# Kernel tuning notes

Measured on AMD Instinct MI355X. Metric: run time of the kernel, lower is better.

The kernel has to match this reference:

```python
import jax, jax.numpy as jnp
import numpy as np

N_NODES = 100000
N_EDGES = 1600000
IN_DIM = 128
HIDDEN = 128
OUT_DIM = 64


def setup_inputs() -> dict:
    key = jax.random.key(0)
    ks = jax.random.split(key, 10)
    s = 0.05
    return {
        "x": jax.random.normal(ks[0], (N_NODES, IN_DIM), jnp.float32),
        "edge_index": jax.random.randint(ks[1], (2, N_EDGES), 0, N_NODES, dtype=jnp.int64),
        "w_l0": jax.random.normal(ks[2], (IN_DIM, HIDDEN), jnp.float32) * s,
        "b_l0": jnp.zeros((HIDDEN,), jnp.float32),
        "w_r0": jax.random.normal(ks[3], (IN_DIM, HIDDEN), jnp.float32) * s,
        "w_l1": jax.random.normal(ks[4], (HIDDEN, HIDDEN), jnp.float32) * s,
        "b_l1": jnp.zeros((HIDDEN,), jnp.float32),
        "w_r1": jax.random.normal(ks[5], (HIDDEN, HIDDEN), jnp.float32) * s,
        "w_out": jax.random.normal(ks[6], (HIDDEN, OUT_DIM), jnp.float32) * s,
        "b_out": jnp.zeros((OUT_DIM,), jnp.float32),
    }


def _sage_conv(x, src, dst, w_l, b_l, w_r, num_nodes):
    # mean-aggregate source features at destination nodes (PyG SAGEConv, aggr='mean')
    msgs = x[src]                                             # [E, D] gather
    agg = jax.ops.segment_sum(msgs, dst, num_segments=num_nodes)
    deg = jax.ops.segment_sum(jnp.ones((src.shape[0],), x.dtype), dst,
                              num_segments=num_nodes)
    agg = agg / jnp.maximum(deg, 1.0)[:, None]                # isolated nodes -> 0
    return agg @ w_l + b_l + x @ w_r


def reference(x, edge_index, w_l0, b_l0, w_r0, w_l1, b_l1, w_r1, w_out, b_out):
    src, dst = edge_index[0], edge_index[1]
    n = x.shape[0]
    h = jax.nn.relu(_sage_conv(x, src, dst, w_l0, b_l0, w_r0, n))
    h = jax.nn.relu(_sage_conv(h, src, dst, w_l1, b_l1, w_r1, n))
    return jax.nn.sigmoid(h @ w_out + b_out)
```

## Files before the change

### kernel.cpp

```cpp
#include <hip/hip_runtime.h>
#include <hip/hip_bf16.h>
#include <cstdint>

#define N_NODES 100000
#define N_EDGES 1600000
#define DIM 128
#define K2 256
#define ODIM 64
#define NPB 64
#define CB 98
#define NREP 8
#define CAP1 2560
#define EPB 4096

typedef __hip_bfloat16 bf16;
typedef __attribute__((ext_vector_type(8))) short bfrag;
typedef __attribute__((ext_vector_type(4))) float f32x4;
typedef __attribute__((ext_vector_type(2))) float f32x2;

__global__ __launch_bounds__(1024) void k_bucket(const int* __restrict__ src,
                                                 const int* __restrict__ dst,
                                                 int* __restrict__ gcur,
                                                 uint32_t* __restrict__ bdata) {
  __shared__ int hist[CB], hbase[CB], hcur[CB], gstart[CB];
  __shared__ uint32_t ent[EPB];
  __shared__ uint8_t kslot[EPB];
  const int tid = threadIdx.x;
  const int rep = blockIdx.x & (NREP - 1);
  const int e0 = blockIdx.x * EPB;
  const int cnt = min(EPB, N_EDGES - e0);

  if (tid < CB) { hist[tid] = 0; hcur[tid] = 0; }
  __syncthreads();

  const int me0 = e0 + tid * 4;
  int ss[4], dd[4];
  int nmine = max(0, min(4, N_EDGES - me0));
  if (nmine == 4) {
    *(int4*)ss = *(const int4*)(src + me0);
    *(int4*)dd = *(const int4*)(dst + me0);
  } else {
    for (int q = 0; q < nmine; ++q) { ss[q] = src[me0 + q]; dd[q] = dst[me0 + q]; }
  }

#pragma unroll
  for (int q = 0; q < 4; ++q)
    if (q < nmine) atomicAdd(&hist[dd[q] >> 10], 1);
  __syncthreads();

  if (tid == 0) {
    int run = 0;
    for (int b = 0; b < CB; ++b) { hbase[b] = run; run += hist[b]; }
  }
  __syncthreads();

#pragma unroll
  for (int q = 0; q < 4; ++q)
    if (q < nmine) {
      int key = dd[q] >> 10;
      int r = atomicAdd(&hcur[key], 1);
      int p = hbase[key] + r;
      ent[p] = ((uint32_t)ss[q] << 10) | (uint32_t)(dd[q] & 1023);
      kslot[p] = (uint8_t)key;
    }
  __syncthreads();

  if (tid < CB && hist[tid] > 0)
    gstart[tid] = atomicAdd(&gcur[rep * CB + tid], hist[tid]);
  __syncthreads();

  for (int i = tid; i < cnt; i += 1024) {
    int k = kslot[i];
    int pos = gstart[k] + (i - hbase[k]);
    if (pos < CAP1)
      bdata[((size_t)(rep * CB + k)) * CAP1 + pos] = ent[i];
  }
}

__global__ __launch_bounds__(256) void k_csr(const uint32_t* __restrict__ bdata,
                                             const int* __restrict__ gcur,
                                             int* __restrict__ rowptr,
                                             int* __restrict__ col) {
  __shared__ int nc[1024], noff[1024];
  __shared__ int red[256];
  __shared__ int sz[NREP];
  const int b = blockIdx.x, tid = threadIdx.x;

  if (tid < NREP) sz[tid] = min(gcur[tid * CB + b], CAP1);

  int part = 0;
  for (int i = tid; i < NREP * b; i += 256) {
    int bp = i >> 3, r = i & 7;
    part += min(gcur[r * CB + bp], CAP1);
  }
  red[tid] = part;
  __syncthreads();
  for (int off = 128; off > 0; off >>= 1) {
    if (tid < off) red[tid] += red[tid + off];
    __syncthreads();
  }
  const int base = red[0];
  __syncthreads();

  for (int i = tid; i < 1024; i += 256) nc[i] = 0;
  __syncthreads();

  for (int r = 0; r < NREP; ++r) {
    int c = sz[r];
    const uint32_t* seg = bdata + ((size_t)(r * CB + b)) * CAP1;
    for (int i = tid; i < c; i += 256)
      atomicAdd(&nc[seg[i] & 1023], 1);
  }
  __syncthreads();

  int loc[4], s = 0;
#pragma unroll
  for (int q = 0; q < 4; ++q) { loc[q] = nc[tid * 4 + q]; s += loc[q]; }
  red[tid] = s;
  __syncthreads();
  for (int off = 1; off < 256; off <<= 1) {
    int add = (tid >= off) ? red[tid - off] : 0;
    __syncthreads();
    red[tid] += add;
    __syncthreads();
  }
  int p = red[tid] - s;
#pragma unroll
  for (int q = 0; q < 4; ++q) { noff[tid * 4 + q] = p; p += loc[q]; }
  __syncthreads();

  for (int i = tid; i < 1024; i += 256) {
    int n = b * 1024 + i;
    if (n < N_NODES) rowptr[n] = base + noff[i];
  }
  if (b == 0 && tid == 0) rowptr[N_NODES] = N_EDGES;

  for (int i = tid; i < 1024; i += 256) nc[i] = 0;
  __syncthreads();

  for (int r = 0; r < NREP; ++r) {
    int c = sz[r];
    const uint32_t* seg = bdata + ((size_t)(r * CB + b)) * CAP1;
    for (int i = tid; i < c; i += 256) {
      uint32_t e = seg[i];
      int n = e & 1023;
      int pos = atomicAdd(&nc[n], 1);
      col[base + noff[n] + pos] = (int)((e >> 10) << 7);
    }
  }
}

__global__ __launch_bounds__(256) void k_cvt(const float* __restrict__ x,
                                             bf16* __restrict__ xb,
                                             uint8_t* __restrict__ x8) {
  int i = (blockIdx.x * 256 + threadIdx.x) * 4;
  if (i >= N_NODES * DIM) return;
  float4 v = *(const float4*)(x + i);
  bf16 t[4];
  t[0] = __float2bfloat16(v.x);
  t[1] = __float2bfloat16(v.y);
  t[2] = __float2bfloat16(v.z);
  t[3] = __float2bfloat16(v.w);
  *(uint2*)(xb + i) = *(uint2*)t;
  int p8 = __builtin_amdgcn_cvt_pk_fp8_f32(v.x, v.y, 0, false);
  p8 = __builtin_amdgcn_cvt_pk_fp8_f32(v.z, v.w, p8, true);
  *(int*)(x8 + i) = p8;
}

__global__ __launch_bounds__(256) void k_cvt8(const bf16* __restrict__ h,
                                              uint8_t* __restrict__ h8) {
  int i = (blockIdx.x * 256 + threadIdx.x) * 8;
  if (i >= N_NODES * DIM) return;
  uint4 v = *(const uint4*)(h + i);
  uint32_t ws[4] = {v.x, v.y, v.z, v.w};
  float f[8];
#pragma unroll
  for (int q = 0; q < 4; ++q) {
    f[2 * q]     = __uint_as_float(ws[q] << 16);
    f[2 * q + 1] = __uint_as_float(ws[q] & 0xFFFF0000u);
  }
  int lo = __builtin_amdgcn_cvt_pk_fp8_f32(f[0], f[1], 0, false);
  lo = __builtin_amdgcn_cvt_pk_fp8_f32(f[2], f[3], lo, true);
  int hi = __builtin_amdgcn_cvt_pk_fp8_f32(f[4], f[5], 0, false);
  hi = __builtin_amdgcn_cvt_pk_fp8_f32(f[6], f[7], hi, true);
  uint2 o; o.x = (uint32_t)lo; o.y = (uint32_t)hi;
  *(uint2*)(h8 + i) = o;
}

__global__ __launch_bounds__(256) void k_prepw(const float* __restrict__ wl0,
                                               const float* __restrict__ wr0,
                                               const float* __restrict__ wl1,
                                               const float* __restrict__ wr1,
                                               const float* __restrict__ wo,
                                               bf16* __restrict__ WT0,
                                               bf16* __restrict__ WT1,
                                               bf16* __restrict__ WoT) {
  int g = blockIdx.x * 256 + threadIdx.x;
  if (g < 32768) {
    int j = g >> 8, k = g & 255;
    float v = (k < DIM) ? wl0[k * DIM + j] : wr0[(k - DIM) * DIM + j];
    WT0[g] = __float2bfloat16(v);
  } else if (g < 65536) {
    int gg = g - 32768;
    int j = gg >> 8, k = gg & 255;
    float v = (k < DIM) ? wl1[k * DIM + j] : wr1[(k - DIM) * DIM + j];
    WT1[gg] = __float2bfloat16(v);
  } else if (g < 65536 + 8192) {
    int gg = g - 65536;
    int j = gg >> 7, k = gg & 127;
    WoT[gg] = __float2bfloat16(wo[k * ODIM + j]);
  }
}

__device__ __forceinline__ void accv8(f32x2* acc, uint2 v) {
  f32x2 t0 = __builtin_amdgcn_cvt_pk_f32_fp8(v.x, false);
  f32x2 t1 = __builtin_amdgcn_cvt_pk_f32_fp8(v.x, true);
  f32x2 t2 = __builtin_amdgcn_cvt_pk_f32_fp8(v.y, false);
  f32x2 t3 = __builtin_amdgcn_cvt_pk_f32_fp8(v.y, true);
  acc[0] += t0; acc[1] += t1; acc[2] += t2; acc[3] += t3;
}

__global__ __launch_bounds__(256) void k_agg(const uint8_t* __restrict__ feat8,
                                             const int* __restrict__ rowptr,
                                             const int* __restrict__ colb,
                                             bf16* __restrict__ agg) {
  int gid = blockIdx.x * 256 + threadIdx.x;
  int node = gid >> 6;
  if (node >= N_NODES) return;
  int lane = gid & 63;
  int g = lane >> 4, lg = lane & 15;
  int beg = rowptr[node], end = rowptr[node + 1];
  const char* fb = (const char*)feat8 + lg * 8;

  f32x2 acc[4];
#pragma unroll
  for (int q = 0; q < 4; ++q) acc[q] = (f32x2){0.f, 0.f};

  int j = beg;
  for (; j + 16 <= end; j += 16) {
    int o0 = colb[j + g];
    int o1 = colb[j + 4 + g];
    int o2 = colb[j + 8 + g];
    int o3 = colb[j + 12 + g];
    uint2 v0 = *(const uint2*)(fb + o0);
    uint2 v1 = *(const uint2*)(fb + o1);
    uint2 v2 = *(const uint2*)(fb + o2);
    uint2 v3 = *(const uint2*)(fb + o3);
    accv8(acc, v0); accv8(acc, v1); accv8(acc, v2); accv8(acc, v3);
  }
  for (; j + 4 <= end; j += 4) {
    int o = colb[j + g];
    uint2 v = *(const uint2*)(fb + o);
    accv8(acc, v);
  }
  int rem = end - j;
  if (g < rem) {
    int o = colb[j + g];
    uint2 v = *(const uint2*)(fb + o);
    accv8(acc, v);
  }

#pragma unroll
  for (int q = 0; q < 4; ++q) {
#pragma unroll
    for (int c = 0; c < 2; ++c) {
      acc[q][c] += __shfl_xor(acc[q][c], 16, 64);
      acc[q][c] += __shfl_xor(acc[q][c], 32, 64);
    }
  }

  if (g == 0) {
    float inv = (end > beg) ? 1.0f / (float)(end - beg) : 0.f;
    union { uint32_t u[4]; uint4 v; } o;
#pragma unroll
    for (int q = 0; q < 4; ++q) {
      __hip_bfloat162 h;
      h.x = __float2bfloat16(acc[q][0] * inv);
      h.y = __float2bfloat16(acc[q][1] * inv);
      o.u[q] = *(uint32_t*)&h;
    }
    *(uint4*)(agg + (size_t)node * DIM + lg * 8) = o.v;
  }
}

__global__ __launch_bounds__(256) void k_sage(const bf16* __restrict__ agg,
                                              const bf16* __restrict__ xb,
                                              const bf16* __restrict__ WT,
                                              const float* __restrict__ bias,
                                              bf16* __restrict__ hout) {
  __shared__ char sA[NPB * 512];
  const int tid = threadIdx.x;
  const int base = blockIdx.x * NPB;

#pragma unroll
  for (int i = 0; i < 8; ++i) {
    int c = tid + 256 * i;
    int row = c >> 5, kc = c & 31;
    int n = base + row;
    uint4 v = make_uint4(0, 0, 0, 0);
    if (n < N_NODES) {
      const bf16* sp = (kc < 16) ? (agg + (size_t)n * DIM + kc * 8)
                                 : (xb + (size_t)n * DIM + (kc - 16) * 8);
      v = *(const uint4*)sp;
    }
    int byte = (row * 512 + kc * 16) ^ ((row & 7) << 4);
    *(uint4*)(sA + byte) = v;
  }
  __syncthreads();

  const int w = tid >> 6, lane = tid & 63;
  const int j0 = w * 32;
  const int lrow = lane & 15, lk = lane >> 4;

  f32x4 acc[4][2];
#pragma unroll
  for (int mi = 0; mi < 4; ++mi)
#pragma unroll
    for (int ni = 0; ni < 2; ++ni)
      acc[mi][ni] = (f32x4){0.f, 0.f, 0.f, 0.f};

  for (int kt = 0; kt < 8; ++kt) {
    bfrag b0 = *(const bfrag*)(WT + (size_t)(j0 + lrow) * K2 + kt * 32 + lk * 8);
    bfrag b1 = *(const bfrag*)(WT + (size_t)(j0 + 16 + lrow) * K2 + kt * 32 + lk * 8);
#pragma unroll
    for (int mi = 0; mi < 4; ++mi) {
      int row = mi * 16 + lrow;
      int byte = (row * 512 + kt * 64 + lk * 16) ^ ((row & 7) << 4);
      bfrag a = *(const bfrag*)(sA + byte);
      acc[mi][0] = __builtin_amdgcn_mfma_f32_16x16x32_bf16(a, b0, acc[mi][0], 0, 0, 0);
      acc[mi][1] = __builtin_amdgcn_mfma_f32_16x16x32_bf16(a, b1, acc[mi][1], 0, 0, 0);
    }
  }

#pragma unroll
  for (int ni = 0; ni < 2; ++ni) {
    int colj = j0 + ni * 16 + lrow;
    float bv = bias[colj];
#pragma unroll
    for (int mi = 0; mi < 4; ++mi) {
#pragma unroll
      for (int r = 0; r < 4; ++r) {
        int n = base + mi * 16 + lk * 4 + r;
        if (n < N_NODES)
          hout[(size_t)n * DIM + colj] = __float2bfloat16(fmaxf(acc[mi][ni][r] + bv, 0.f));
      }
    }
  }
}

__global__ __launch_bounds__(256) void k_out(const bf16* __restrict__ agg,
                                             const bf16* __restrict__ xb,
                                             const bf16* __restrict__ WT,
                                             const float* __restrict__ bias,
                                             const bf16* __restrict__ WoT,
                                             const float* __restrict__ bo,
                                             float* __restrict__ out) {
  __shared__ char sA[NPB * 512];
  const int tid = threadIdx.x;
  const int base = blockIdx.x * NPB;

#pragma unroll
  for (int i = 0; i < 8; ++i) {
    int c = tid + 256 * i;
    int row = c >> 5, kc = c & 31;
    int n = base + row;
    uint4 v = make_uint4(0, 0, 0, 0);
    if (n < N_NODES) {
      const bf16* sp = (kc < 16) ? (agg + (size_t)n * DIM + kc * 8)
                                 : (xb + (size_t)n * DIM + (kc - 16) * 8);
      v = *(const uint4*)sp;
    }
    int byte = (row * 512 + kc * 16) ^ ((row & 7) << 4);
    *(uint4*)(sA + byte) = v;
  }
  __syncthreads();

  const int w = tid >> 6, lane = tid & 63;
  const int j0 = w * 32;
  const int lrow = lane & 15, lk = lane >> 4;

  f32x4 acc[4][2];
#pragma unroll
  for (int mi = 0; mi < 4; ++mi)
#pragma unroll
    for (int ni = 0; ni < 2; ++ni)
      acc[mi][ni] = (f32x4){0.f, 0.f, 0.f, 0.f};

  for (int kt = 0; kt < 8; ++kt) {
    bfrag b0 = *(const bfrag*)(WT + (size_t)(j0 + lrow) * K2 + kt * 32 + lk * 8);
    bfrag b1 = *(const bfrag*)(WT + (size_t)(j0 + 16 + lrow) * K2 + kt * 32 + lk * 8);
#pragma unroll
    for (int mi = 0; mi < 4; ++mi) {
      int row = mi * 16 + lrow;
      int byte = (row * 512 + kt * 64 + lk * 16) ^ ((row & 7) << 4);
      bfrag a = *(const bfrag*)(sA + byte);
      acc[mi][0] = __builtin_amdgcn_mfma_f32_16x16x32_bf16(a, b0, acc[mi][0], 0, 0, 0);
      acc[mi][1] = __builtin_amdgcn_mfma_f32_16x16x32_bf16(a, b1, acc[mi][1], 0, 0, 0);
    }
  }

  __syncthreads();
#pragma unroll
  for (int ni = 0; ni < 2; ++ni) {
    int colj = j0 + ni * 16 + lrow;
    float bv = bias[colj];
#pragma unroll
    for (int mi = 0; mi < 4; ++mi) {
#pragma unroll
      for (int r = 0; r < 4; ++r) {
        int row = mi * 16 + lk * 4 + r;
        float v = fmaxf(acc[mi][ni][r] + bv, 0.f);
        int byte = (row * 256 + colj * 2) ^ ((row & 7) << 4);
        *(bf16*)(sA + byte) = __float2bfloat16(v);
      }
    }
  }
  __syncthreads();

  const int jo = w * 16;
  f32x4 acc2[4];
#pragma unroll
  for (int mi = 0; mi < 4; ++mi) acc2[mi] = (f32x4){0.f, 0.f, 0.f, 0.f};

#pragma unroll
  for (int kt = 0; kt < 4; ++kt) {
    bfrag b = *(const bfrag*)(WoT + (size_t)(jo + lrow) * DIM + kt * 32 + lk * 8);
#pragma unroll
    for (int mi = 0; mi < 4; ++mi) {
      int row = mi * 16 + lrow;
      int byte = (row * 256 + kt * 64 + lk * 16) ^ ((row & 7) << 4);
      bfrag a = *(const bfrag*)(sA + byte);
      acc2[mi] = __builtin_amdgcn_mfma_f32_16x16x32_bf16(a, b, acc2[mi], 0, 0, 0);
    }
  }

  int colj = jo + lrow;
  float bv = bo[colj];
#pragma unroll
  for (int mi = 0; mi < 4; ++mi) {
#pragma unroll
    for (int r = 0; r < 4; ++r) {
      int n = base + mi * 16 + lk * 4 + r;
      if (n < N_NODES)
        out[(size_t)n * ODIM + colj] = 1.f / (1.f + __expf(-(acc2[mi][r] + bv)));
    }
  }
}

extern "C" void kernel_launch(void* const* d_in, const int* in_sizes, int n_in,
                              void* d_out, int out_size, void* d_ws, size_t ws_size,
                              hipStream_t stream) {
  const float* x     = (const float*)d_in[0];
  const int*   ei    = (const int*)d_in[1];
  const float* w_l0  = (const float*)d_in[2];
  const float* b_l0  = (const float*)d_in[3];
  const float* w_r0  = (const float*)d_in[4];
  const float* w_l1  = (const float*)d_in[5];
  const float* b_l1  = (const float*)d_in[6];
  const float* w_r1  = (const float*)d_in[7];
  const float* w_out = (const float*)d_in[8];
  const float* b_out = (const float*)d_in[9];
  float* out = (float*)d_out;

  const int* src = ei;
  const int* dst = ei + N_EDGES;

  char* ws = (char*)d_ws;
  int*      rowptr = (int*)(ws);
  int*      gcur   = (int*)(ws + (512u << 10));
  int*      col    = (int*)(ws + (1u << 20));
  uint32_t* bdata  = (uint32_t*)(ws + (8u << 20));
  uint8_t*  x8     = (uint8_t*)(ws + (8u << 20));
  uint8_t*  h08    = (uint8_t*)(ws + (8u << 20));
  bf16*     WT0    = (bf16*)(ws + (21u << 20));
  bf16*     WT1    = (bf16*)(ws + (21u << 20) + 65536);
  bf16*     WoT    = (bf16*)(ws + (21u << 20) + 131072);
  bf16*     aggb   = (bf16*)(ws + (22ull << 20));
  bf16*     h0b    = (bf16*)(ws + (48ull << 20));
  bf16*     xb     = (bf16*)(ws + (74ull << 20));

  hipMemsetAsync(gcur, 0, NREP * CB * sizeof(int), stream);
  k_bucket<<<(N_EDGES + EPB - 1) / EPB, 1024, 0, stream>>>(src, dst, gcur, bdata);
  k_csr   <<<CB, 256, 0, stream>>>(bdata, gcur, rowptr, col);

  k_cvt  <<<(N_NODES * DIM / 4 + 255) / 256, 256, 0, stream>>>(x, xb, x8);
  k_prepw<<<(65536 + 8192 + 255) / 256, 256, 0, stream>>>(w_l0, w_r0, w_l1, w_r1, w_out,
                                                          WT0, WT1, WoT);

  const int ablocks = (N_NODES * 64 + 255) / 256;
  const int gblocks = (N_NODES + NPB - 1) / NPB;

  k_agg <<<ablocks, 256, 0, stream>>>(x8, rowptr, col, aggb);
  k_sage<<<gblocks, 256, 0, stream>>>(aggb, xb, WT0, b_l0, h0b);

  k_cvt8<<<(N_NODES * DIM / 8 + 255) / 256, 256, 0, stream>>>(h0b, h08);
  k_agg <<<ablocks, 256, 0, stream>>>(h08, rowptr, col, aggb);
  k_out <<<gblocks, 256, 0, stream>>>(aggb, h0b, WT1, b_l1, WoT, b_out, out);
}
```

Before: 238.8 us.

## Fuse fp8 conversion into sage epilogue, use direct LDS loads, per-wave histograms

Removes the separate k_cvt8 kernel by having k_sage write the fp8 copy of the hidden layer alongside the bf16 output. The A-tile staging in k_sage and k_out now uses global_load_lds to copy straight into shared memory, folding the XOR swizzle into the source address. k_bucket switches to per-wave histograms and cursors to reduce LDS atomic contention. The trade-offs are byte-wide scattered fp8 stores in the epilogue and clamped duplicate loads for tail rows.

```diff
diff --git a/kernel.cpp b/kernel.cpp
--- a/kernel.cpp
+++ b/kernel.cpp
@@ -12,25 +12,37 @@
 #define NREP 8
 #define CAP1 2560
 #define EPB 4096
+#define NWAVE 16
 
 typedef __hip_bfloat16 bf16;
 typedef __attribute__((ext_vector_type(8))) short bfrag;
 typedef __attribute__((ext_vector_type(4))) float f32x4;
 typedef __attribute__((ext_vector_type(2))) float f32x2;
 
+__device__ __forceinline__ void gload16(const void* g, void* l) {
+  __builtin_amdgcn_global_load_lds((const __attribute__((address_space(1))) void*)g,
+                                   (__attribute__((address_space(3))) void*)l, 16, 0, 0);
+}
+
 __global__ __launch_bounds__(1024) void k_bucket(const int* __restrict__ src,
                                                  const int* __restrict__ dst,
                                                  int* __restrict__ gcur,
                                                  uint32_t* __restrict__ bdata) {
-  __shared__ int hist[CB], hbase[CB], hcur[CB], gstart[CB];
+  __shared__ int wh[NWAVE][CB];
+  __shared__ int wcur[NWAVE][CB];
+  __shared__ int hist[CB], hbase[CB], gstart[CB];
   __shared__ uint32_t ent[EPB];
   __shared__ uint8_t kslot[EPB];
   const int tid = threadIdx.x;
+  const int wave = tid >> 6;
   const int rep = blockIdx.x & (NREP - 1);
   const int e0 = blockIdx.x * EPB;
   const int cnt = min(EPB, N_EDGES - e0);
 
-  if (tid < CB) { hist[tid] = 0; hcur[tid] = 0; }
+  for (int i = tid; i < NWAVE * CB; i += 1024) {
+    ((int*)wh)[i] = 0;
+    ((int*)wcur)[i] = 0;
+  }
   __syncthreads();
 
   const int me0 = e0 + tid * 4;
@@ -45,7 +57,19 @@
 
 #pragma unroll
   for (int q = 0; q < 4; ++q)
-    if (q < nmine) atomicAdd(&hist[dd[q] >> 10], 1);
+    if (q < nmine) atomicAdd(&wh[wave][dd[q] >> 10], 1);
+  __syncthreads();
+
+  if (tid < CB) {
+    int run = 0;
+#pragma unroll
+    for (int w = 0; w < NWAVE; ++w) {
+      int c = wh[w][tid];
+      wh[w][tid] = run;
+      run += c;
+    }
+    hist[tid] = run;
+  }
   __syncthreads();
 
   if (tid == 0) {
@@ -58,8 +82,8 @@
   for (int q = 0; q < 4; ++q)
     if (q < nmine) {
       int key = dd[q] >> 10;
-      int r = atomicAdd(&hcur[key], 1);
-      int p = hbase[key] + r;
+      int r = atomicAdd(&wcur[wave][key], 1);
+      int p = hbase[key] + wh[wave][key] + r;
       ent[p] = ((uint32_t)ss[q] << 10) | (uint32_t)(dd[q] & 1023);
       kslot[p] = (uint8_t)key;
     }
@@ -165,26 +189,6 @@
   int p8 = __builtin_amdgcn_cvt_pk_fp8_f32(v.x, v.y, 0, false);
   p8 = __builtin_amdgcn_cvt_pk_fp8_f32(v.z, v.w, p8, true);
   *(int*)(x8 + i) = p8;
-}
-
-__global__ __launch_bounds__(256) void k_cvt8(const bf16* __restrict__ h,
-                                              uint8_t* __restrict__ h8) {
-  int i = (blockIdx.x * 256 + threadIdx.x) * 8;
-  if (i >= N_NODES * DIM) return;
-  uint4 v = *(const uint4*)(h + i);
-  uint32_t ws[4] = {v.x, v.y, v.z, v.w};
-  float f[8];
-#pragma unroll
-  for (int q = 0; q < 4; ++q) {
-    f[2 * q]     = __uint_as_float(ws[q] << 16);
-    f[2 * q + 1] = __uint_as_float(ws[q] & 0xFFFF0000u);
-  }
-  int lo = __builtin_amdgcn_cvt_pk_fp8_f32(f[0], f[1], 0, false);
-  lo = __builtin_amdgcn_cvt_pk_fp8_f32(f[2], f[3], lo, true);
-  int hi = __builtin_amdgcn_cvt_pk_fp8_f32(f[4], f[5], 0, false);
-  hi = __builtin_amdgcn_cvt_pk_fp8_f32(f[6], f[7], hi, true);
-  uint2 o; o.x = (uint32_t)lo; o.y = (uint32_t)hi;
-  *(uint2*)(h8 + i) = o;
 }
 
 __global__ __launch_bounds__(256) void k_prepw(const float* __restrict__ wl0,
@@ -287,7 +291,8 @@
                                               const bf16* __restrict__ xb,
                                               const bf16* __restrict__ WT,
                                               const float* __restrict__ bias,
-                                              bf16* __restrict__ hout) {
+                                              bf16* __restrict__ hout,
+                                              uint8_t* __restrict__ h8) {
   __shared__ char sA[NPB * 512];
   const int tid = threadIdx.x;
   const int base = blockIdx.x * NPB;
@@ -295,16 +300,12 @@
 #pragma unroll
   for (int i = 0; i < 8; ++i) {
     int c = tid + 256 * i;
-    int row = c >> 5, kc = c & 31;
-    int n = base + row;
-    uint4 v = make_uint4(0, 0, 0, 0);
-    if (n < N_NODES) {
-      const bf16* sp = (kc < 16) ? (agg + (size_t)n * DIM + kc * 8)
-                                 : (xb + (size_t)n * DIM + (kc - 16) * 8);
-      v = *(const uint4*)sp;
-    }
-    int byte = (row * 512 + kc * 16) ^ ((row & 7) << 4);
-    *(uint4*)(sA + byte) = v;
+    int row = c >> 5;
+    int n = min(base + row, N_NODES - 1);
+    int kcg = (c & 31) ^ (row & 7);
+    const bf16* sp = (kcg < 16) ? (agg + (size_t)n * DIM + kcg * 8)
+                                : (xb + (size_t)n * DIM + (kcg - 16) * 8);
+    gload16(sp, sA + c * 16);
   }
   __syncthreads();
 
@@ -341,8 +342,12 @@
 #pragma unroll
       for (int r = 0; r < 4; ++r) {
         int n = base + mi * 16 + lk * 4 + r;
-        if (n < N_NODES)
-          hout[(size_t)n * DIM + colj] = __float2bfloat16(fmaxf(acc[mi][ni][r] + bv, 0.f));
+        if (n < N_NODES) {
+          float v = fmaxf(acc[mi][ni][r] + bv, 0.f);
+          hout[(size_t)n * DIM + colj] = __float2bfloat16(v);
+          h8[(size_t)n * DIM + colj] =
+              (uint8_t)(__builtin_amdgcn_cvt_pk_fp8_f32(v, v, 0, false) & 0xFF);
+        }
       }
     }
   }
@@ -362,16 +367,12 @@
 #pragma unroll
   for (int i = 0; i < 8; ++i) {
     int c = tid + 256 * i;
-    int row = c >> 5, kc = c & 31;
-    int n = base + row;
-    uint4 v = make_uint4(0, 0, 0, 0);
-    if (n < N_NODES) {
-      const bf16* sp = (kc < 16) ? (agg + (size_t)n * DIM + kc * 8)
-                                 : (xb + (size_t)n * DIM + (kc - 16) * 8);
-      v = *(const uint4*)sp;
-    }
-    int byte = (row * 512 + kc * 16) ^ ((row & 7) << 4);
-    *(uint4*)(sA + byte) = v;
+    int row = c >> 5;
+    int n = min(base + row, N_NODES - 1);
+    int kcg = (c & 31) ^ (row & 7);
+    const bf16* sp = (kcg < 16) ? (agg + (size_t)n * DIM + kcg * 8)
+                                : (xb + (size_t)n * DIM + (kcg - 16) * 8);
+    gload16(sp, sA + c * 16);
   }
   __syncthreads();
 
@@ -491,9 +492,8 @@
   const int gblocks = (N_NODES + NPB - 1) / NPB;
 
   k_agg <<<ablocks, 256, 0, stream>>>(x8, rowptr, col, aggb);
-  k_sage<<<gblocks, 256, 0, stream>>>(aggb, xb, WT0, b_l0, h0b);
-
-  k_cvt8<<<(N_NODES * DIM / 8 + 255) / 256, 256, 0, stream>>>(h0b, h08);
-  k_agg <<<ablocks, 256, 0, stream>>>(h08, rowptr, col, aggb);
-  k_out <<<gblocks, 256, 0, stream>>>(aggb, h0b, WT1, b_l1, WoT, b_out, out);
-}
+  k_sage<<<gblocks, 256, 0, stream>>>(aggb, xb, WT0, b_l0, h0b, h08);
+
+  k_agg<<<ablocks, 256, 0, stream>>>(h08, rowptr, col, aggb);
+  k_out<<<gblocks, 256, 0, stream>>>(aggb, h0b, WT1, b_l1, WoT, b_out, out);
+}
```

New measurement: 233.2 us. 1.02x faster.
